# Performance work log

Measured on AMD Instinct MI355X. Metric: run time of the kernel, lower is better.

Reference implementation:

```python
import jax, jax.numpy as jnp
import numpy as np

D_MODEL = 1024
D_HEAD = 128


def setup_inputs() -> dict:
    key = jax.random.key(0)
    kx, kq, kk, kv, ko = jax.random.split(key, 5)
    x = jax.random.normal(kx, (4, 2048, D_MODEL), dtype=jnp.float32)
    # xavier-uniform-ish init scale
    s_in = (6.0 / (D_MODEL + D_HEAD)) ** 0.5
    wq = jax.random.uniform(kq, (D_MODEL, D_HEAD), minval=-s_in, maxval=s_in, dtype=jnp.float32)
    wk = jax.random.uniform(kk, (D_MODEL, D_HEAD), minval=-s_in, maxval=s_in, dtype=jnp.float32)
    wv = jax.random.uniform(kv, (D_MODEL, D_HEAD), minval=-s_in, maxval=s_in, dtype=jnp.float32)
    wo = jax.random.uniform(ko, (D_HEAD, D_MODEL), minval=-s_in, maxval=s_in, dtype=jnp.float32)
    return {"x": x, "wq": wq, "wk": wk, "wv": wv, "wo": wo}


def reference(x, wq, wk, wv, wo):
    # x: [b, s, d_model]
    s = x.shape[1]
    scale = 1.0 / (D_HEAD ** 0.5)
    q = jnp.einsum('bsd,dh->bsh', x, wq)
    k = jnp.einsum('bsd,dh->bsh', x, wk)
    v = jnp.einsum('bsd,dh->bsh', x, wv)
    scores = jnp.einsum('bqh,bkh->bqk', q, k) * scale  # [b, s, s]
    causal = jnp.tril(jnp.ones((s, s), dtype=bool))
    scores = jnp.where(causal, scores, -jnp.inf)
    attn = jax.nn.softmax(scores, axis=-1)
    ctx = jnp.einsum('bqk,bkh->bqh', attn, v)
    return jnp.einsum('bsh,hd->bsd', ctx, wo)
```

## Files before the change

kernel.cpp:

```cpp
#include <hip/hip_runtime.h>
#include <hip/hip_bf16.h>
#include <math.h>

typedef _Float16 half8 __attribute__((ext_vector_type(8)));
typedef _Float16 half4_t __attribute__((ext_vector_type(4)));
typedef _Float16 half2_t __attribute__((ext_vector_type(2)));
typedef float floatx4 __attribute__((ext_vector_type(4)));
typedef float floatx2 __attribute__((ext_vector_type(2)));

#define MFMA16(a, b, c) __builtin_amdgcn_mfma_f32_16x16x32_f16(a, b, c, 0, 0, 0)
#define MASKVAL (-30000.0f)
#define QSCALE 0.1275261529f

__global__ __launch_bounds__(256) void wprep(
    const float* __restrict__ wq, const float* __restrict__ wk,
    const float* __restrict__ wv, const float* __restrict__ wo,
    _Float16* __restrict__ wqt, _Float16* __restrict__ wkt,
    _Float16* __restrict__ wvt, _Float16* __restrict__ wot) {
  __shared__ float T[32][36];
  int bx = blockIdx.x, tid = threadIdx.x;
  const float* src;
  _Float16* dst;
  int R, C, r0, c0;
  float sc = 1.0f;
  if (bx < 384) {
    int p = bx >> 7, t = bx & 127;
    src = (p == 0) ? wq : (p == 1) ? wk : wv;
    dst = (p == 0) ? wqt : (p == 1) ? wkt : wvt;
    if (p == 0) sc = QSCALE;
    R = 1024; C = 128;
    r0 = (t & 31) * 32; c0 = (t >> 5) * 32;
  } else {
    int t = bx - 384;
    src = wo; dst = wot;
    R = 128; C = 1024;
    r0 = (t & 3) * 32; c0 = (t >> 2) * 32;
  }
  {
    int row = tid >> 3, c4 = (tid & 7) * 4;
    float4 f = *(const float4*)&src[(size_t)(r0 + row) * C + c0 + c4];
    T[row][c4] = f.x; T[row][c4 + 1] = f.y; T[row][c4 + 2] = f.z; T[row][c4 + 3] = f.w;
  }
  __syncthreads();
  {
    int cc = tid >> 3, r4 = (tid & 7) * 4;
    half4_t h;
    h[0] = (_Float16)(T[r4 + 0][cc] * sc);
    h[1] = (_Float16)(T[r4 + 1][cc] * sc);
    h[2] = (_Float16)(T[r4 + 2][cc] * sc);
    h[3] = (_Float16)(T[r4 + 3][cc] * sc);
    *(half4_t*)&dst[(size_t)(c0 + cc) * R + r0 + r4] = h;
  }
}

__global__ __launch_bounds__(512, 4) void qkv_fused(
    const float* __restrict__ x, const _Float16* __restrict__ wqt,
    const _Float16* __restrict__ wkt, const _Float16* __restrict__ wvt,
    _Float16* __restrict__ Qh, _Float16* __restrict__ Kh,
    _Float16* __restrict__ Vt) {
  __shared__ _Float16 A_lds[16 * 72];
  __shared__ _Float16 B_lds[384 * 72];
  int tid = threadIdx.x;
  int w = tid >> 6, lane = tid & 63, quad = lane >> 4, l16 = lane & 15;
  int m0 = blockIdx.x * 16;
  floatx4 zero = {0.f, 0.f, 0.f, 0.f};
  floatx4 acc[3];
#pragma unroll
  for (int ni = 0; ni < 3; ni++) acc[ni] = zero;

  int arow = tid >> 5, ac0 = (tid & 31) * 2;
  int brow = tid >> 2, bc0 = (tid & 3) * 16;

  const float* asrc = x + (size_t)(m0 + arow) * 1024 + ac0;
  const _Float16* bsrc0 = wqt + (size_t)brow * 1024 + bc0;
  const _Float16* bsrc1 = wkt + (size_t)brow * 1024 + bc0;
  const _Float16* bsrc2 = wvt + (size_t)brow * 1024 + bc0;

  float2 af;
  half8 bf[3][2];
  af = *(const float2*)asrc;
#pragma unroll
  for (int i = 0; i < 2; i++) {
    bf[0][i] = *(const half8*)(bsrc0 + i * 8);
    bf[1][i] = *(const half8*)(bsrc1 + i * 8);
    bf[2][i] = *(const half8*)(bsrc2 + i * 8);
  }

  for (int k0 = 0; k0 < 1024; k0 += 64) {
    {
      half2_t h;
      h[0] = (_Float16)af.x; h[1] = (_Float16)af.y;
      *(half2_t*)&A_lds[arow * 72 + ac0] = h;
    }
#pragma unroll
    for (int p = 0; p < 3; p++)
#pragma unroll
      for (int i = 0; i < 2; i++)
        *(half8*)&B_lds[(p * 128 + brow) * 72 + bc0 + i * 8] = bf[p][i];
    __syncthreads();

    if (k0 + 64 < 1024) {
      af = *(const float2*)(asrc + k0 + 64);
#pragma unroll
      for (int i = 0; i < 2; i++) {
        bf[0][i] = *(const half8*)(bsrc0 + k0 + 64 + i * 8);
        bf[1][i] = *(const half8*)(bsrc1 + k0 + 64 + i * 8);
        bf[2][i] = *(const half8*)(bsrc2 + k0 + 64 + i * 8);
      }
    }

    half8 a[2];
#pragma unroll
    for (int kc = 0; kc < 2; kc++)
      a[kc] = *(const half8*)&A_lds[l16 * 72 + kc * 32 + quad * 8];
    int nw = w * 48;
#pragma unroll
    for (int ni = 0; ni < 3; ni++)
#pragma unroll
      for (int kc = 0; kc < 2; kc++) {
        half8 b = *(const half8*)&B_lds[(nw + ni * 16 + l16) * 72 + kc * 32 + quad * 8];
        acc[ni] = MFMA16(a[kc], b, acc[ni]);
      }
    __syncthreads();
  }

  _Float16* Vl = B_lds;
#pragma unroll
  for (int ni = 0; ni < 3; ni++) {
    int nb = w * 48 + ni * 16;
#pragma unroll
    for (int r = 0; r < 4; r++) {
      int row = m0 + quad * 4 + r;
      _Float16 v = (_Float16)acc[ni][r];
      if (nb < 128)
        Qh[(size_t)row * 128 + nb + l16] = v;
      else if (nb < 256)
        Kh[(size_t)row * 128 + nb - 128 + l16] = v;
      else
        Vl[(nb - 256 + l16) * 24 + quad * 4 + r] = v;
    }
  }
  __syncthreads();
  if (tid < 256) {
    int col = tid >> 1, hh = tid & 1;
    int bb = m0 >> 11, s0 = (m0 & 2047) + hh * 8;
    half8 h0 = *(half8*)&Vl[col * 24 + hh * 8];
    *(half8*)&Vt[((size_t)(bb * 128 + col)) * 2048 + s0] = h0;
  }
}

__global__ __launch_bounds__(256, 3) void attn_partial(
    const _Float16* __restrict__ Qh, const _Float16* __restrict__ Kh,
    const _Float16* __restrict__ Vt, _Float16* __restrict__ Opart,
    float* __restrict__ Ml) {
  __shared__ _Float16 KV_lds[128 * 136];
  __shared__ _Float16 P_lds[4 * 16 * 136];
  int tid = threadIdx.x;
  int w = tid >> 6, lane = tid & 63, quad = lane >> 4, l16 = lane & 15;
  int g = (int)blockIdx.x;
  int b = g & 3;
  int r = g >> 2;
  int m = (int)sqrtf((float)r * 0.5f);
  while (2 * m * (m + 1) > r) m--;
  while (2 * (m + 1) * (m + 2) <= r) m++;
  int r0_ = r - 2 * m * (m + 1);
  int qdiv = r0_ / (m + 1);
  int qt = 4 * m + qdiv;
  int kc = r0_ - qdiv * (m + 1);
  int q0 = qt * 64, k0 = kc * 256;
  int kmax = (qt + 1) * 64;
  int len = kmax - k0; if (len > 256) len = 256;
  int nsub = (len + 127) >> 7;
  int qw0 = q0 + w * 16;
  int sidx = (b * 32 + qt) * 8 + kc;

  const _Float16* Kb = Kh + (size_t)b * 2048 * 128;
  const _Float16* Vb = Vt + (size_t)b * 128 * 2048;

  half8 aq[4];
  {
    const _Float16* qbase = Qh + (size_t)(b * 2048 + qw0 + l16) * 128;
#pragma unroll
    for (int c = 0; c < 4; c++) aq[c] = *(const half8*)&qbase[c * 32 + quad * 8];
  }

  int srow = tid >> 1, scol = (tid & 1) * 64;
  floatx4 zero = {0.f, 0.f, 0.f, 0.f};
  floatx4 O[8];
#pragma unroll
  for (int t = 0; t < 8; t++) O[t] = zero;
  float m_r[4] = {MASKVAL, MASKVAL, MASKVAL, MASKVAL};
  float l_r[4] = {0.f, 0.f, 0.f, 0.f};

  for (int s = 0; s < nsub; s++) {
    int ks = k0 + s * 128;
    if (s) __syncthreads();
#pragma unroll
    for (int i = 0; i < 8; i++)
      *(half8*)&KV_lds[srow * 136 + scol + i * 8] =
          *(const half8*)&Kb[(size_t)(ks + srow) * 128 + scol + i * 8];
    half8 vreg[8];
#pragma unroll
    for (int i = 0; i < 8; i++)
      vreg[i] = *(const half8*)&Vb[(size_t)srow * 2048 + ks + scol + i * 8];
    __syncthreads();

    floatx4 sa[8];
#pragma unroll
    for (int t = 0; t < 8; t++) sa[t] = zero;
#pragma unroll
    for (int t = 0; t < 8; t++)
#pragma unroll
      for (int c = 0; c < 4; c++) {
        half8 bk = *(const half8*)&KV_lds[(t * 16 + l16) * 136 + c * 32 + quad * 8];
        sa[t] = MFMA16(aq[c], bk, sa[t]);
      }

    float sc[4];
#pragma unroll
    for (int j = 0; j < 4; j++) {
      int query = qw0 + quad * 4 + j;
      float mx = MASKVAL;
#pragma unroll
      for (int t = 0; t < 8; t++) {
        float v = (ks + t * 16 + l16 > query) ? MASKVAL : sa[t][j];
        sa[t][j] = v;
        mx = fmaxf(mx, v);
      }
#pragma unroll
      for (int off = 1; off < 16; off <<= 1) mx = fmaxf(mx, __shfl_xor(mx, off));
      float mnew = fmaxf(m_r[j], mx);
      float scj = exp2f(m_r[j] - mnew);
      float rs = 0.f;
#pragma unroll
      for (int t = 0; t < 8; t++) {
        float e = exp2f(sa[t][j] - mnew);
        sa[t][j] = e;
        rs += e;
      }
#pragma unroll
      for (int off = 1; off < 16; off <<= 1) rs += __shfl_xor(rs, off);
      l_r[j] = l_r[j] * scj + rs;
      m_r[j] = mnew;
      sc[j] = scj;
    }
#pragma unroll
    for (int t = 0; t < 8; t++)
#pragma unroll
      for (int j = 0; j < 4; j++) O[t][j] *= sc[j];

    __syncthreads();
#pragma unroll
    for (int i = 0; i < 8; i++)
      *(half8*)&KV_lds[srow * 136 + scol + i * 8] = vreg[i];
    _Float16* P = P_lds + w * 16 * 136;
#pragma unroll
    for (int j = 0; j < 4; j++)
#pragma unroll
      for (int t = 0; t < 8; t++)
        P[(quad * 4 + j) * 136 + t * 16 + l16] = (_Float16)sa[t][j];
    __syncthreads();

#pragma unroll
    for (int c2 = 0; c2 < 4; c2++) {
      half8 ap = *(const half8*)&P[l16 * 136 + c2 * 32 + quad * 8];
#pragma unroll
      for (int t = 0; t < 8; t++) {
        half8 bv = *(const half8*)&KV_lds[(t * 16 + l16) * 136 + c2 * 32 + quad * 8];
        O[t] = MFMA16(ap, bv, O[t]);
      }
    }
  }

  size_t obase = (size_t)sidx * 8192;
#pragma unroll
  for (int t = 0; t < 8; t++)
#pragma unroll
    for (int j = 0; j < 4; j++)
      Opart[obase + (size_t)(w * 16 + quad * 4 + j) * 128 + t * 16 + l16] = (_Float16)O[t][j];
  if (l16 == 0)
#pragma unroll
    for (int j = 0; j < 4; j++) {
      int row = w * 16 + quad * 4 + j;
      floatx2 ml;
      ml[0] = m_r[j];
      ml[1] = l_r[j];
      *(floatx2*)&Ml[(size_t)sidx * 128 + row * 2] = ml;
    }
}

__global__ __launch_bounds__(512, 2) void combine_out(
    const _Float16* __restrict__ Opart, const float* __restrict__ Ml,
    const _Float16* __restrict__ wot, float* __restrict__ out) {
  __shared__ _Float16 A_lds[32 * 136];
  __shared__ _Float16 B_lds[128 * 136];
  int tid = threadIdx.x;
  int r0 = blockIdx.x * 32;
  int b = r0 >> 11, s0 = r0 & 2047;
  int qt = s0 >> 6, rbase = s0 & 63;
  int nkc = (qt + 4) >> 2;
  int sidx0 = (b * 32 + qt) * 8;

  {
    int lr = tid >> 4, c0 = (tid & 15) * 8;
    int ri = rbase + lr;
    float mv[8], lv[8];
#pragma unroll
    for (int i = 0; i < 8; i++) {
      if (i < nkc) {
        floatx2 ml = *(const floatx2*)&Ml[(size_t)(sidx0 + i) * 128 + ri * 2];
        mv[i] = ml[0]; lv[i] = ml[1];
      } else { mv[i] = MASKVAL; lv[i] = 0.f; }
    }
    float M = MASKVAL;
#pragma unroll
    for (int i = 0; i < 8; i++) M = fmaxf(M, mv[i]);
    float L = 0.f;
    float a0[8];
#pragma unroll
    for (int c = 0; c < 8; c++) a0[c] = 0.f;
#pragma unroll
    for (int i = 0; i < 8; i++) {
      if (i < nkc) {
        float scv = exp2f(mv[i] - M);
        L += lv[i] * scv;
        half8 o0 = *(const half8*)&Opart[(size_t)(sidx0 + i) * 8192 + (size_t)ri * 128 + c0];
#pragma unroll
        for (int c = 0; c < 8; c++) a0[c] += scv * (float)o0[c];
      }
    }
    float inv = 1.f / L;
    half8 h0;
#pragma unroll
    for (int c = 0; c < 8; c++) h0[c] = (_Float16)(a0[c] * inv);
    *(half8*)&A_lds[lr * 136 + c0] = h0;
  }

  int w = tid >> 6, lane = tid & 63, quad = lane >> 4, l16 = lane & 15;
  int bn = tid >> 2, bk = (tid & 3) * 32;
  half8 bf[4];
#pragma unroll
  for (int i = 0; i < 4; i++)
    bf[i] = *(const half8*)&wot[(size_t)bn * 128 + bk + i * 8];
  __syncthreads();

  half8 a[2][4];
#pragma unroll
  for (int c = 0; c < 4; c++) {
    a[0][c] = *(const half8*)&A_lds[l16 * 136 + c * 32 + quad * 8];
    a[1][c] = *(const half8*)&A_lds[(16 + l16) * 136 + c * 32 + quad * 8];
  }
  floatx4 zero = {0.f, 0.f, 0.f, 0.f};
  for (int nc = 0; nc < 8; nc++) {
#pragma unroll
    for (int i = 0; i < 4; i++)
      *(half8*)&B_lds[bn * 136 + bk + i * 8] = bf[i];
    __syncthreads();
    if (nc < 7) {
#pragma unroll
      for (int i = 0; i < 4; i++)
        bf[i] = *(const half8*)&wot[(size_t)((nc + 1) * 128 + bn) * 128 + bk + i * 8];
    }
    floatx4 acc[2];
    acc[0] = zero; acc[1] = zero;
    int nw = w * 16;
#pragma unroll
    for (int c = 0; c < 4; c++) {
      half8 bb2 = *(const half8*)&B_lds[(nw + l16) * 136 + c * 32 + quad * 8];
      acc[0] = MFMA16(a[0][c], bb2, acc[0]);
      acc[1] = MFMA16(a[1][c], bb2, acc[1]);
    }
#pragma unroll
    for (int mi = 0; mi < 2; mi++)
#pragma unroll
      for (int r = 0; r < 4; r++) {
        int row = r0 + mi * 16 + quad * 4 + r;
        out[(size_t)row * 1024 + nc * 128 + nw + l16] = acc[mi][r];
      }
    __syncthreads();
  }
}

extern "C" void kernel_launch(void* const* d_in, const int* in_sizes, int n_in,
                              void* d_out, int out_size, void* d_ws, size_t ws_size,
                              hipStream_t stream) {
  const float* x = (const float*)d_in[0];
  const float* wq = (const float*)d_in[1];
  const float* wk = (const float*)d_in[2];
  const float* wv = (const float*)d_in[3];
  const float* wo = (const float*)d_in[4];
  char* ws = (char*)d_ws;
  _Float16* wqt = (_Float16*)(ws + 0);
  _Float16* wkt = (_Float16*)(ws + 262144);
  _Float16* wvt = (_Float16*)(ws + 524288);
  _Float16* wot = (_Float16*)(ws + 786432);
  _Float16* Qh  = (_Float16*)(ws + 1048576);
  _Float16* Kh  = (_Float16*)(ws + 3145728);
  _Float16* Vt  = (_Float16*)(ws + 5242880);
  _Float16* Opart = (_Float16*)(ws + 9437184);
  float* Ml = (float*)(ws + 26214400);
  float* out = (float*)d_out;

  wprep<<<512, 256, 0, stream>>>(wq, wk, wv, wo, wqt, wkt, wvt, wot);
  qkv_fused<<<512, 512, 0, stream>>>(x, wqt, wkt, wvt, Qh, Kh, Vt);
  attn_partial<<<576, 256, 0, stream>>>(Qh, Kh, Vt, Opart, Ml);
  combine_out<<<256, 512, 0, stream>>>(Opart, Ml, wot, out);
}
```

Before: 147.4 us.

## Double QKV row tile and widen attention key chunks to 512

The QKV projection kernel now computes 32 rows per block instead of 16, so each loaded weight tile feeds two MFMA row groups. This halves the grid and the redundant weight traffic. The attention split-K scheme moves from 256-key chunks with a sqrt-based tile mapping to 512-key chunks with an explicit longest-first block order, giving fewer partial results for the combine kernel to merge. The trade-off is fewer blocks in both kernels, which may leave CUs idle or unbalanced, and more accumulator registers in the projection.

Measured after the change: 152.3 us. 1.03x slower.

```diff
diff --git a/kernel.cpp b/kernel.cpp
--- a/kernel.cpp
+++ b/kernel.cpp
@@ -58,17 +58,19 @@
     const _Float16* __restrict__ wkt, const _Float16* __restrict__ wvt,
     _Float16* __restrict__ Qh, _Float16* __restrict__ Kh,
     _Float16* __restrict__ Vt) {
-  __shared__ _Float16 A_lds[16 * 72];
+  __shared__ _Float16 A_lds[32 * 72];
   __shared__ _Float16 B_lds[384 * 72];
   int tid = threadIdx.x;
   int w = tid >> 6, lane = tid & 63, quad = lane >> 4, l16 = lane & 15;
-  int m0 = blockIdx.x * 16;
+  int m0 = blockIdx.x * 32;
   floatx4 zero = {0.f, 0.f, 0.f, 0.f};
-  floatx4 acc[3];
-#pragma unroll
-  for (int ni = 0; ni < 3; ni++) acc[ni] = zero;
-
-  int arow = tid >> 5, ac0 = (tid & 31) * 2;
+  floatx4 acc[2][3];
+#pragma unroll
+  for (int mi = 0; mi < 2; mi++)
+#pragma unroll
+    for (int ni = 0; ni < 3; ni++) acc[mi][ni] = zero;
+
+  int arow = tid >> 4, ac0 = (tid & 15) * 4;
   int brow = tid >> 2, bc0 = (tid & 3) * 16;
 
   const float* asrc = x + (size_t)(m0 + arow) * 1024 + ac0;
@@ -76,9 +78,9 @@
   const _Float16* bsrc1 = wkt + (size_t)brow * 1024 + bc0;
   const _Float16* bsrc2 = wvt + (size_t)brow * 1024 + bc0;
 
-  float2 af;
+  float4 af;
   half8 bf[3][2];
-  af = *(const float2*)asrc;
+  af = *(const float4*)asrc;
 #pragma unroll
   for (int i = 0; i < 2; i++) {
     bf[0][i] = *(const half8*)(bsrc0 + i * 8);
@@ -88,9 +90,10 @@
 
   for (int k0 = 0; k0 < 1024; k0 += 64) {
     {
-      half2_t h;
+      half4_t h;
       h[0] = (_Float16)af.x; h[1] = (_Float16)af.y;
-      *(half2_t*)&A_lds[arow * 72 + ac0] = h;
+      h[2] = (_Float16)af.z; h[3] = (_Float16)af.w;
+      *(half4_t*)&A_lds[arow * 72 + ac0] = h;
     }
 #pragma unroll
     for (int p = 0; p < 3; p++)
@@ -100,7 +103,7 @@
     __syncthreads();
 
     if (k0 + 64 < 1024) {
-      af = *(const float2*)(asrc + k0 + 64);
+      af = *(const float4*)(asrc + k0 + 64);
 #pragma unroll
       for (int i = 0; i < 2; i++) {
         bf[0][i] = *(const half8*)(bsrc0 + k0 + 64 + i * 8);
@@ -109,43 +112,51 @@
       }
     }
 
-    half8 a[2];
-#pragma unroll
-    for (int kc = 0; kc < 2; kc++)
-      a[kc] = *(const half8*)&A_lds[l16 * 72 + kc * 32 + quad * 8];
+    half8 a[2][2];
+#pragma unroll
+    for (int mi = 0; mi < 2; mi++)
+#pragma unroll
+      for (int kc = 0; kc < 2; kc++)
+        a[mi][kc] = *(const half8*)&A_lds[(mi * 16 + l16) * 72 + kc * 32 + quad * 8];
     int nw = w * 48;
 #pragma unroll
     for (int ni = 0; ni < 3; ni++)
 #pragma unroll
       for (int kc = 0; kc < 2; kc++) {
         half8 b = *(const half8*)&B_lds[(nw + ni * 16 + l16) * 72 + kc * 32 + quad * 8];
-        acc[ni] = MFMA16(a[kc], b, acc[ni]);
+        acc[0][ni] = MFMA16(a[0][kc], b, acc[0][ni]);
+        acc[1][ni] = MFMA16(a[1][kc], b, acc[1][ni]);
       }
     __syncthreads();
   }
 
   _Float16* Vl = B_lds;
 #pragma unroll
-  for (int ni = 0; ni < 3; ni++) {
-    int nb = w * 48 + ni * 16;
-#pragma unroll
-    for (int r = 0; r < 4; r++) {
-      int row = m0 + quad * 4 + r;
-      _Float16 v = (_Float16)acc[ni][r];
-      if (nb < 128)
-        Qh[(size_t)row * 128 + nb + l16] = v;
-      else if (nb < 256)
-        Kh[(size_t)row * 128 + nb - 128 + l16] = v;
-      else
-        Vl[(nb - 256 + l16) * 24 + quad * 4 + r] = v;
-    }
-  }
+  for (int mi = 0; mi < 2; mi++)
+#pragma unroll
+    for (int ni = 0; ni < 3; ni++) {
+      int nb = w * 48 + ni * 16;
+#pragma unroll
+      for (int r = 0; r < 4; r++) {
+        int row = m0 + mi * 16 + quad * 4 + r;
+        _Float16 v = (_Float16)acc[mi][ni][r];
+        if (nb < 128)
+          Qh[(size_t)row * 128 + nb + l16] = v;
+        else if (nb < 256)
+          Kh[(size_t)row * 128 + nb - 128 + l16] = v;
+        else
+          Vl[(nb - 256 + l16) * 40 + mi * 16 + quad * 4 + r] = v;
+      }
+    }
   __syncthreads();
   if (tid < 256) {
     int col = tid >> 1, hh = tid & 1;
-    int bb = m0 >> 11, s0 = (m0 & 2047) + hh * 8;
-    half8 h0 = *(half8*)&Vl[col * 24 + hh * 8];
-    *(half8*)&Vt[((size_t)(bb * 128 + col)) * 2048 + s0] = h0;
+    int bb = m0 >> 11, s0 = (m0 & 2047) + hh * 16;
+    half8 h0 = *(half8*)&Vl[col * 40 + hh * 16];
+    half8 h1 = *(half8*)&Vl[col * 40 + hh * 16 + 8];
+    _Float16* dstv = Vt + ((size_t)(bb * 128 + col)) * 2048 + s0;
+    *(half8*)&dstv[0] = h0;
+    *(half8*)&dstv[8] = h1;
   }
 }
 
@@ -160,19 +171,18 @@
   int g = (int)blockIdx.x;
   int b = g & 3;
   int r = g >> 2;
-  int m = (int)sqrtf((float)r * 0.5f);
-  while (2 * m * (m + 1) > r) m--;
-  while (2 * (m + 1) * (m + 2) <= r) m++;
-  int r0_ = r - 2 * m * (m + 1);
-  int qdiv = r0_ / (m + 1);
-  int qt = 4 * m + qdiv;
-  int kc = r0_ - qdiv * (m + 1);
-  int q0 = qt * 64, k0 = kc * 256;
+  int qt, kc;
+  if (r < 32)      { qt = 31 - (r >> 2); kc = r & 3; }
+  else if (r < 56) { int rr = r - 32; int d = rr / 3;
+                     qt = 23 - d; kc = rr - d * 3; }
+  else if (r < 72) { int rr = r - 56; qt = 15 - (rr >> 1); kc = rr & 1; }
+  else             { qt = 7 - (r - 72); kc = 0; }
+  int q0 = qt * 64, k0 = kc * 512;
   int kmax = (qt + 1) * 64;
-  int len = kmax - k0; if (len > 256) len = 256;
+  int len = kmax - k0; if (len > 512) len = 512;
   int nsub = (len + 127) >> 7;
   int qw0 = q0 + w * 16;
-  int sidx = (b * 32 + qt) * 8 + kc;
+  int sidx = (b * 32 + qt) * 4 + kc;
 
   const _Float16* Kb = Kh + (size_t)b * 2048 * 128;
   const _Float16* Vb = Vt + (size_t)b * 128 * 2048;
@@ -298,15 +308,15 @@
   int r0 = blockIdx.x * 32;
   int b = r0 >> 11, s0 = r0 & 2047;
   int qt = s0 >> 6, rbase = s0 & 63;
-  int nkc = (qt + 4) >> 2;
-  int sidx0 = (b * 32 + qt) * 8;
+  int nkc = (qt + 8) >> 3;
+  int sidx0 = (b * 32 + qt) * 4;
 
   {
     int lr = tid >> 4, c0 = (tid & 15) * 8;
     int ri = rbase + lr;
-    float mv[8], lv[8];
-#pragma unroll
-    for (int i = 0; i < 8; i++) {
+    float mv[4], lv[4];
+#pragma unroll
+    for (int i = 0; i < 4; i++) {
       if (i < nkc) {
         floatx2 ml = *(const floatx2*)&Ml[(size_t)(sidx0 + i) * 128 + ri * 2];
         mv[i] = ml[0]; lv[i] = ml[1];
@@ -314,13 +324,13 @@
     }
     float M = MASKVAL;
 #pragma unroll
-    for (int i = 0; i < 8; i++) M = fmaxf(M, mv[i]);
+    for (int i = 0; i < 4; i++) M = fmaxf(M, mv[i]);
     float L = 0.f;
     float a0[8];
 #pragma unroll
     for (int c = 0; c < 8; c++) a0[c] = 0.f;
 #pragma unroll
-    for (int i = 0; i < 8; i++) {
+    for (int i = 0; i < 4; i++) {
       if (i < nkc) {
         float scv = exp2f(mv[i] - M);
         L += lv[i] * scv;
@@ -398,11 +408,11 @@
   _Float16* Kh  = (_Float16*)(ws + 3145728);
   _Float16* Vt  = (_Float16*)(ws + 5242880);
   _Float16* Opart = (_Float16*)(ws + 9437184);
-  float* Ml = (float*)(ws + 26214400);
+  float* Ml = (float*)(ws + 17825792);
   float* out = (float*)d_out;
 
   wprep<<<512, 256, 0, stream>>>(wq, wk, wv, wo, wqt, wkt, wvt, wot);
-  qkv_fused<<<512, 512, 0, stream>>>(x, wqt, wkt, wvt, Qh, Kh, Vt);
-  attn_partial<<<576, 256, 0, stream>>>(Qh, Kh, Vt, Opart, Ml);
+  qkv_fused<<<256, 512, 0, stream>>>(x, wqt, wkt, wvt, Qh, Kh, Vt);
+  attn_partial<<<320, 256, 0, stream>>>(Qh, Kh, Vt, Opart, Ml);
   combine_out<<<256, 512, 0, stream>>>(Opart, Ml, wot, out);
 }
```
